# Kernel optimization log

Hardware: AMD Instinct MI355X
Metric: run time of the kernel (lower is better)

Reference implementation:

```python
import jax, jax.numpy as jnp
import numpy as np

BN_EPS = 1e-5


def setup_inputs() -> dict:
    key = jax.random.key(0)
    k1, k2, k3, k4, k5 = jax.random.split(key, 5)
    B, M, N = 4, 65536, 16384
    C_pre, C_cur, D_out = 64, 128, 128
    C_in = C_pre + C_cur  # 192
    pre_x = jax.random.normal(k1, (B, C_pre, M), dtype=jnp.float32)
    cur_x = jax.random.normal(k2, (B, C_cur, N), dtype=jnp.float32)
    up_idx = jax.random.randint(k3, (B, M, 1), 0, N, dtype=jnp.int64)
    w = jax.random.normal(k4, (C_in, D_out), dtype=jnp.float32) * 0.05
    b = jax.random.normal(k5, (D_out,), dtype=jnp.float32) * 0.05
    gamma = jnp.ones((D_out,), dtype=jnp.float32)
    beta = jnp.zeros((D_out,), dtype=jnp.float32)
    run_mean = jnp.zeros((D_out,), dtype=jnp.float32)
    run_var = jnp.ones((D_out,), dtype=jnp.float32)
    return {"pre_x": pre_x, "cur_x": cur_x, "up_idx": up_idx, "w": w, "b": b,
            "gamma": gamma, "beta": beta, "run_mean": run_mean, "run_var": run_var}


def reference(pre_x, cur_x, up_idx, w, b, gamma, beta, run_mean, run_var):
    # indexing_neighbor(cur_x.permute(0,2,1), up_idx).squeeze(2):
    # gather coarse-point features at nearest-neighbor indices -> [B, C_cur, M]
    idx = up_idx[:, :, 0]                                   # [B, M]
    feat = jnp.take_along_axis(cur_x, idx[:, None, :], axis=2)  # [B, C_cur, M]
    x = jnp.concatenate([pre_x, feat], axis=1)              # [B, C_in, M]
    # ConvTranspose1d(kernel=1) == pointwise linear with weight [C_in, D_out]
    y = jnp.einsum('bcm,cd->bdm', x, w) + b[None, :, None]  # [B, D_out, M]
    # BatchNorm1d (inference form with running stats) + ReLU
    inv = jax.lax.rsqrt(run_var + BN_EPS)
    y = (y - run_mean[None, :, None]) * (inv * gamma)[None, :, None] + beta[None, :, None]
    y = jnp.maximum(y, 0.0)
    return y.transpose(0, 2, 1)                             # [B, M, D_out]
```

## Files before the change

### kernel.cpp

```cpp
#include <hip/hip_runtime.h>
#include <hip/hip_bf16.h>


typedef short bhalf8 __attribute__((ext_vector_type(8)));
typedef float f32x4 __attribute__((ext_vector_type(4)));
typedef unsigned int u32x4 __attribute__((ext_vector_type(4)));

__device__ __forceinline__ short f2bf(float f) {
  unsigned int u = __float_as_uint(f);
  unsigned int r = (u + 0x7fffu + ((u >> 16) & 1u)) >> 16;
  return (short)r;
}

__global__ __launch_bounds__(256) void transpose_cur(const float* __restrict__ cur,
                                                     short* __restrict__ curT) {
  __shared__ float tile[128][65];
  const int b = blockIdx.y;
  const int n0 = blockIdx.x << 6;
  const float* src = cur + (size_t)b * 128 * 16384;
#pragma unroll
  for (int it = 0; it < 8; ++it) {
    int v = it * 256 + threadIdx.x;
    int cc = v >> 4;
    int nq = (v & 15) << 2;
    f32x4 f = __builtin_nontemporal_load(
        reinterpret_cast<const f32x4*>(&src[(size_t)cc * 16384 + n0 + nq]));
    tile[cc][nq + 0] = f[0];
    tile[cc][nq + 1] = f[1];
    tile[cc][nq + 2] = f[2];
    tile[cc][nq + 3] = f[3];
  }
  __syncthreads();
  short* dst = curT + ((size_t)b * 16384 + n0) * 128;
#pragma unroll
  for (int it = 0; it < 4; ++it) {
    int v = it * 256 + threadIdx.x;
    int nn = v >> 4;
    int c8 = (v & 15) << 3;
    bhalf8 pk;
#pragma unroll
    for (int j = 0; j < 8; ++j) pk[j] = f2bf(tile[c8 + j][nn]);
    *reinterpret_cast<bhalf8*>(&dst[(size_t)nn * 128 + c8]) = pk;
  }
}

#define NBLK 2048

__global__ __launch_bounds__(256, 3) void fused_gemm(
    const float* __restrict__ pre_x,
    const int* __restrict__ up_idx,
    const float* __restrict__ w,
    const float* __restrict__ bias,
    const float* __restrict__ gamma, const float* __restrict__ beta,
    const float* __restrict__ rmean, const float* __restrict__ rvar,
    const short* __restrict__ curT,
    float* __restrict__ out)
{
  __shared__ short x_lds[64 * 200];
  const int tid = threadIdx.x;
  const int lane = tid & 63;
  const int wv = tid >> 6;
  const int c = lane & 15;
  const int g = lane >> 4;

  bhalf8 bf[6][2];
#pragma unroll
  for (int s = 0; s < 6; ++s)
#pragma unroll
    for (int ct = 0; ct < 2; ++ct) {
      const int col = 32 * wv + 16 * ct + c;
#pragma unroll
      for (int j = 0; j < 8; ++j)
        bf[s][ct][j] = f2bf(w[(32 * s + 8 * g + j) * 128 + col]);
    }

  float scale[2], shift[2];
#pragma unroll
  for (int ct = 0; ct < 2; ++ct) {
    const int d = 32 * wv + 16 * ct + c;
    float sc = gamma[d] * rsqrtf(rvar[d] + 1e-5f);
    scale[ct] = sc;
    shift[ct] = (bias[d] - rmean[d]) * sc + beta[d];
  }

  for (int t = 0; t < 2; ++t) {
    const long rg = blockIdx.x + (long)t * NBLK;
    const long r0 = rg << 6;
    const int b = (int)(r0 >> 16);
    const int m0 = (int)(r0 & 65535);
    if (t) __syncthreads();

    {
      const float* pb = pre_x + (size_t)b * 64 * 65536 + m0;
#pragma unroll
      for (int it = 0; it < 4; ++it) {
        int v = it * 256 + tid;
        int cc = v >> 4;
        int mq = (v & 15) << 2;
        f32x4 f = __builtin_nontemporal_load(
            reinterpret_cast<const f32x4*>(&pb[(size_t)cc * 65536 + mq]));
        x_lds[(mq + 0) * 200 + cc] = f2bf(f[0]);
        x_lds[(mq + 1) * 200 + cc] = f2bf(f[1]);
        x_lds[(mq + 2) * 200 + cc] = f2bf(f[2]);
        x_lds[(mq + 3) * 200 + cc] = f2bf(f[3]);
      }
    }
    {
#pragma unroll
      for (int it = 0; it < 4; ++it) {
        int mm = it * 16 + (tid >> 4);
        int seg = tid & 15;
        int n = up_idx[r0 + mm];
        const short* srcp = curT + ((size_t)b * 16384 + n) * 128 + seg * 8;
        *reinterpret_cast<u32x4*>(&x_lds[mm * 200 + 64 + seg * 8]) =
            *reinterpret_cast<const u32x4*>(srcp);
      }
    }
    __syncthreads();

#pragma unroll
    for (int rt = 0; rt < 4; ++rt) {
      bhalf8 a[6];
#pragma unroll
      for (int s = 0; s < 6; ++s)
        a[s] = *reinterpret_cast<const bhalf8*>(
            &x_lds[(16 * rt + c) * 200 + 32 * s + 8 * g]);
      f32x4 acc0 = {0.f, 0.f, 0.f, 0.f};
      f32x4 acc1 = {0.f, 0.f, 0.f, 0.f};
#pragma unroll
      for (int s = 0; s < 6; ++s) {
        acc0 = __builtin_amdgcn_mfma_f32_16x16x32_bf16(a[s], bf[s][0], acc0, 0, 0, 0);
        acc1 = __builtin_amdgcn_mfma_f32_16x16x32_bf16(a[s], bf[s][1], acc1, 0, 0, 0);
      }
      float* ob = out + (size_t)(r0 + 16 * rt + 4 * g) * 128 + 32 * wv;
#pragma unroll
      for (int i = 0; i < 4; ++i) {
        float v0 = fmaxf(acc0[i] * scale[0] + shift[0], 0.f);
        float v1 = fmaxf(acc1[i] * scale[1] + shift[1], 0.f);
        __builtin_nontemporal_store(v0, ob + (size_t)i * 128 + c);
        __builtin_nontemporal_store(v1, ob + (size_t)i * 128 + 16 + c);
      }
    }
  }
}

extern "C" void kernel_launch(void* const* d_in, const int* in_sizes, int n_in,
                              void* d_out, int out_size, void* d_ws, size_t ws_size,
                              hipStream_t stream) {
  const float* pre_x = (const float*)d_in[0];
  const float* cur_x = (const float*)d_in[1];
  const int* up_idx = (const int*)d_in[2];
  const float* w = (const float*)d_in[3];
  const float* bias = (const float*)d_in[4];
  const float* gamma = (const float*)d_in[5];
  const float* beta = (const float*)d_in[6];
  const float* rmean = (const float*)d_in[7];
  const float* rvar = (const float*)d_in[8];
  float* out = (float*)d_out;
  short* curT = (short*)d_ws;

  hipLaunchKernelGGL(transpose_cur, dim3(256, 4), dim3(256), 0, stream, cur_x, curT);
  hipLaunchKernelGGL(fused_gemm, dim3(NBLK), dim3(256), 0, stream, pre_x, up_idx, w,
                     bias, gamma, beta, rmean, rvar, curT, out);
}
```

Measured before the change: 233.9 us.

## Prefetch second tile into registers and vectorize output stores via swapped MFMA operands

Loads both tiles' indices up front and prefetches the second tile's pre_x and gathered rows into registers while the first tile computes. Swaps the MFMA A/B operands so each lane holds four consecutive output channels, which allows 16-byte vector nontemporal stores in place of scalar ones. BN scale/shift become per-lane vectors to match. Occupancy hint drops from 3 to 2 blocks per CU to make room for the extra prefetch registers.

```diff
diff --git a/kernel.cpp b/kernel.cpp
--- a/kernel.cpp
+++ b/kernel.cpp
@@ -1,5 +1,4 @@
 #include <hip/hip_runtime.h>
-#include <hip/hip_bf16.h>
 
 
 typedef short bhalf8 __attribute__((ext_vector_type(8)));
@@ -46,7 +45,7 @@
 
 #define NBLK 2048
 
-__global__ __launch_bounds__(256, 3) void fused_gemm(
+__global__ __launch_bounds__(256, 2) void fused_gemm(
     const float* __restrict__ pre_x,
     const int* __restrict__ up_idx,
     const float* __restrict__ w,
@@ -62,6 +61,8 @@
   const int wv = tid >> 6;
   const int c = lane & 15;
   const int g = lane >> 4;
+  const int mrow = tid >> 4;
+  const int seg = tid & 15;
 
   bhalf8 bf[6][2];
 #pragma unroll
@@ -74,50 +75,77 @@
         bf[s][ct][j] = f2bf(w[(32 * s + 8 * g + j) * 128 + col]);
     }
 
-  float scale[2], shift[2];
+  f32x4 scale4[2], shift4[2];
 #pragma unroll
   for (int ct = 0; ct < 2; ++ct) {
-    const int d = 32 * wv + 16 * ct + c;
-    float sc = gamma[d] * rsqrtf(rvar[d] + 1e-5f);
-    scale[ct] = sc;
-    shift[ct] = (bias[d] - rmean[d]) * sc + beta[d];
-  }
-
-  for (int t = 0; t < 2; ++t) {
-    const long rg = blockIdx.x + (long)t * NBLK;
-    const long r0 = rg << 6;
-    const int b = (int)(r0 >> 16);
-    const int m0 = (int)(r0 & 65535);
-    if (t) __syncthreads();
-
-    {
-      const float* pb = pre_x + (size_t)b * 64 * 65536 + m0;
-#pragma unroll
-      for (int it = 0; it < 4; ++it) {
-        int v = it * 256 + tid;
-        int cc = v >> 4;
-        int mq = (v & 15) << 2;
-        f32x4 f = __builtin_nontemporal_load(
-            reinterpret_cast<const f32x4*>(&pb[(size_t)cc * 65536 + mq]));
-        x_lds[(mq + 0) * 200 + cc] = f2bf(f[0]);
-        x_lds[(mq + 1) * 200 + cc] = f2bf(f[1]);
-        x_lds[(mq + 2) * 200 + cc] = f2bf(f[2]);
-        x_lds[(mq + 3) * 200 + cc] = f2bf(f[3]);
-      }
+    const int d0 = 32 * wv + 16 * ct + 4 * g;
+    f32x4 gm = *reinterpret_cast<const f32x4*>(&gamma[d0]);
+    f32x4 rv = *reinterpret_cast<const f32x4*>(&rvar[d0]);
+    f32x4 bs = *reinterpret_cast<const f32x4*>(&bias[d0]);
+    f32x4 rm = *reinterpret_cast<const f32x4*>(&rmean[d0]);
+    f32x4 bt = *reinterpret_cast<const f32x4*>(&beta[d0]);
+#pragma unroll
+    for (int i = 0; i < 4; ++i) {
+      float sc = gm[i] * rsqrtf(rv[i] + 1e-5f);
+      scale4[ct][i] = sc;
+      shift4[ct][i] = (bs[i] - rm[i]) * sc + bt[i];
     }
-    {
-#pragma unroll
-      for (int it = 0; it < 4; ++it) {
-        int mm = it * 16 + (tid >> 4);
-        int seg = tid & 15;
-        int n = up_idx[r0 + mm];
-        const short* srcp = curT + ((size_t)b * 16384 + n) * 128 + seg * 8;
-        *reinterpret_cast<u32x4*>(&x_lds[mm * 200 + 64 + seg * 8]) =
-            *reinterpret_cast<const u32x4*>(srcp);
-      }
-    }
-    __syncthreads();
-
+  }
+
+  const long r0a = ((long)blockIdx.x) << 6;
+  const long r0b = ((long)(blockIdx.x + NBLK)) << 6;
+  const int ba = (int)(r0a >> 16), m0a = (int)(r0a & 65535);
+  const int bb = (int)(r0b >> 16), m0b = (int)(r0b & 65535);
+
+  int idx0[4], idx1[4];
+#pragma unroll
+  for (int it = 0; it < 4; ++it) idx0[it] = up_idx[r0a + it * 16 + mrow];
+#pragma unroll
+  for (int it = 0; it < 4; ++it) idx1[it] = up_idx[r0b + it * 16 + mrow];
+
+  f32x4 pre0[4];
+  const float* pba = pre_x + (size_t)ba * 64 * 65536 + m0a;
+#pragma unroll
+  for (int it = 0; it < 4; ++it)
+    pre0[it] = __builtin_nontemporal_load(reinterpret_cast<const f32x4*>(
+        &pba[(size_t)(it * 16 + mrow) * 65536 + (seg << 2)]));
+  u32x4 gat0[4];
+#pragma unroll
+  for (int it = 0; it < 4; ++it)
+    gat0[it] = *reinterpret_cast<const u32x4*>(
+        curT + ((size_t)ba * 16384 + idx0[it]) * 128 + seg * 8);
+
+#define STAGE_LDS(pre, gat)                                                   \
+  {                                                                           \
+    _Pragma("unroll") for (int it = 0; it < 4; ++it) {                        \
+      const int cc = it * 16 + mrow;                                          \
+      const int mq = seg << 2;                                                \
+      x_lds[(mq + 0) * 200 + cc] = f2bf(pre[it][0]);                          \
+      x_lds[(mq + 1) * 200 + cc] = f2bf(pre[it][1]);                          \
+      x_lds[(mq + 2) * 200 + cc] = f2bf(pre[it][2]);                          \
+      x_lds[(mq + 3) * 200 + cc] = f2bf(pre[it][3]);                          \
+    }                                                                         \
+    _Pragma("unroll") for (int it = 0; it < 4; ++it) {                        \
+      const int mm = it * 16 + mrow;                                          \
+      *reinterpret_cast<u32x4*>(&x_lds[mm * 200 + 64 + seg * 8]) = gat[it];   \
+    }                                                                         \
+  }
+
+  STAGE_LDS(pre0, gat0);
+
+  f32x4 pre1[4];
+  const float* pbb = pre_x + (size_t)bb * 64 * 65536 + m0b;
+#pragma unroll
+  for (int it = 0; it < 4; ++it)
+    pre1[it] = __builtin_nontemporal_load(reinterpret_cast<const f32x4*>(
+        &pbb[(size_t)(it * 16 + mrow) * 65536 + (seg << 2)]));
+  u32x4 gat1[4];
+#pragma unroll
+  for (int it = 0; it < 4; ++it)
+    gat1[it] = *reinterpret_cast<const u32x4*>(
+        curT + ((size_t)bb * 16384 + idx1[it]) * 128 + seg * 8);
+
+  auto compute_tile = [&](long r0) {
 #pragma unroll
     for (int rt = 0; rt < 4; ++rt) {
       bhalf8 a[6];
@@ -129,19 +157,27 @@
       f32x4 acc1 = {0.f, 0.f, 0.f, 0.f};
 #pragma unroll
       for (int s = 0; s < 6; ++s) {
-        acc0 = __builtin_amdgcn_mfma_f32_16x16x32_bf16(a[s], bf[s][0], acc0, 0, 0, 0);
-        acc1 = __builtin_amdgcn_mfma_f32_16x16x32_bf16(a[s], bf[s][1], acc1, 0, 0, 0);
+        acc0 = __builtin_amdgcn_mfma_f32_16x16x32_bf16(bf[s][0], a[s], acc0, 0, 0, 0);
+        acc1 = __builtin_amdgcn_mfma_f32_16x16x32_bf16(bf[s][1], a[s], acc1, 0, 0, 0);
       }
-      float* ob = out + (size_t)(r0 + 16 * rt + 4 * g) * 128 + 32 * wv;
+      float* ob = out + (size_t)(r0 + 16 * rt + c) * 128 + 32 * wv + 4 * g;
+      f32x4 v0, v1;
 #pragma unroll
       for (int i = 0; i < 4; ++i) {
-        float v0 = fmaxf(acc0[i] * scale[0] + shift[0], 0.f);
-        float v1 = fmaxf(acc1[i] * scale[1] + shift[1], 0.f);
-        __builtin_nontemporal_store(v0, ob + (size_t)i * 128 + c);
-        __builtin_nontemporal_store(v1, ob + (size_t)i * 128 + 16 + c);
+        v0[i] = fmaxf(acc0[i] * scale4[0][i] + shift4[0][i], 0.f);
+        v1[i] = fmaxf(acc1[i] * scale4[1][i] + shift4[1][i], 0.f);
       }
+      __builtin_nontemporal_store(v0, reinterpret_cast<f32x4*>(ob));
+      __builtin_nontemporal_store(v1, reinterpret_cast<f32x4*>(ob + 16));
     }
-  }
+  };
+
+  __syncthreads();
+  compute_tile(r0a);
+  __syncthreads();
+  STAGE_LDS(pre1, gat1);
+  __syncthreads();
+  compute_tile(r0b);
 }
 
 extern "C" void kernel_launch(void* const* d_in, const int* in_sizes, int n_in,
```

Measured after the change: 255.6 us. 9.3% more time.

## Vectorize output stores via swapped MFMA operands, fold BN scale into weights, prefetch loads

Applied to the files above, without the earlier changes.

Swaps the A/B operands of the MFMA so each lane holds four consecutive output channels of one row, which allows 16-byte nontemporal stores instead of scalar stores. The BN scale is folded into the bf16 weights so the epilogue becomes a single add and ReLU. Index loads for both tiles are hoisted to the start, and the pre_x and gather loads are issued before any LDS writes to overlap memory latency. Occupancy hint is raised to 4 waves per SIMD, and folding the scale before bf16 rounding slightly changes numerics.

```diff
diff --git a/kernel.cpp b/kernel.cpp
--- a/kernel.cpp
+++ b/kernel.cpp
@@ -1,5 +1,4 @@
 #include <hip/hip_runtime.h>
-#include <hip/hip_bf16.h>
 
 
 typedef short bhalf8 __attribute__((ext_vector_type(8)));
@@ -46,7 +45,7 @@
 
 #define NBLK 2048
 
-__global__ __launch_bounds__(256, 3) void fused_gemm(
+__global__ __launch_bounds__(256, 4) void fused_gemm(
     const float* __restrict__ pre_x,
     const int* __restrict__ up_idx,
     const float* __restrict__ w,
@@ -62,6 +61,15 @@
   const int wv = tid >> 6;
   const int c = lane & 15;
   const int g = lane >> 4;
+  const int mrow = tid >> 4;
+  const int seg = tid & 15;
+
+  float scc[2];
+#pragma unroll
+  for (int ct = 0; ct < 2; ++ct) {
+    const int d = 32 * wv + 16 * ct + c;
+    scc[ct] = gamma[d] * rsqrtf(rvar[d] + 1e-5f);
+  }
 
   bhalf8 bf[6][2];
 #pragma unroll
@@ -71,51 +79,63 @@
       const int col = 32 * wv + 16 * ct + c;
 #pragma unroll
       for (int j = 0; j < 8; ++j)
-        bf[s][ct][j] = f2bf(w[(32 * s + 8 * g + j) * 128 + col]);
+        bf[s][ct][j] = f2bf(w[(32 * s + 8 * g + j) * 128 + col] * scc[ct]);
     }
 
-  float scale[2], shift[2];
+  f32x4 shift4[2];
 #pragma unroll
   for (int ct = 0; ct < 2; ++ct) {
-    const int d = 32 * wv + 16 * ct + c;
-    float sc = gamma[d] * rsqrtf(rvar[d] + 1e-5f);
-    scale[ct] = sc;
-    shift[ct] = (bias[d] - rmean[d]) * sc + beta[d];
+    const int d0 = 32 * wv + 16 * ct + 4 * g;
+    f32x4 gm = *reinterpret_cast<const f32x4*>(&gamma[d0]);
+    f32x4 rv = *reinterpret_cast<const f32x4*>(&rvar[d0]);
+    f32x4 bs = *reinterpret_cast<const f32x4*>(&bias[d0]);
+    f32x4 rm = *reinterpret_cast<const f32x4*>(&rmean[d0]);
+    f32x4 bt = *reinterpret_cast<const f32x4*>(&beta[d0]);
+#pragma unroll
+    for (int i = 0; i < 4; ++i) {
+      float sc = gm[i] * rsqrtf(rv[i] + 1e-5f);
+      shift4[ct][i] = (bs[i] - rm[i]) * sc + bt[i];
+    }
+  }
+
+  int idxp[2][4];
+#pragma unroll
+  for (int t = 0; t < 2; ++t) {
+    const long rr = ((long)(blockIdx.x + t * NBLK)) << 6;
+#pragma unroll
+    for (int it = 0; it < 4; ++it) idxp[t][it] = up_idx[rr + it * 16 + mrow];
   }
 
   for (int t = 0; t < 2; ++t) {
-    const long rg = blockIdx.x + (long)t * NBLK;
-    const long r0 = rg << 6;
+    const long r0 = ((long)(blockIdx.x + t * NBLK)) << 6;
     const int b = (int)(r0 >> 16);
     const int m0 = (int)(r0 & 65535);
     if (t) __syncthreads();
 
-    {
-      const float* pb = pre_x + (size_t)b * 64 * 65536 + m0;
+    const float* pb = pre_x + (size_t)b * 64 * 65536 + m0;
+    f32x4 pr[4];
 #pragma unroll
-      for (int it = 0; it < 4; ++it) {
-        int v = it * 256 + tid;
-        int cc = v >> 4;
-        int mq = (v & 15) << 2;
-        f32x4 f = __builtin_nontemporal_load(
-            reinterpret_cast<const f32x4*>(&pb[(size_t)cc * 65536 + mq]));
-        x_lds[(mq + 0) * 200 + cc] = f2bf(f[0]);
-        x_lds[(mq + 1) * 200 + cc] = f2bf(f[1]);
-        x_lds[(mq + 2) * 200 + cc] = f2bf(f[2]);
-        x_lds[(mq + 3) * 200 + cc] = f2bf(f[3]);
-      }
+    for (int it = 0; it < 4; ++it)
+      pr[it] = __builtin_nontemporal_load(reinterpret_cast<const f32x4*>(
+          &pb[(size_t)(it * 16 + mrow) * 65536 + (seg << 2)]));
+    u32x4 gt[4];
+#pragma unroll
+    for (int it = 0; it < 4; ++it)
+      gt[it] = *reinterpret_cast<const u32x4*>(
+          curT + ((size_t)b * 16384 + idxp[t][it]) * 128 + seg * 8);
+#pragma unroll
+    for (int it = 0; it < 4; ++it) {
+      const int cc = it * 16 + mrow;
+      const int mq = seg << 2;
+      x_lds[(mq + 0) * 200 + cc] = f2bf(pr[it][0]);
+      x_lds[(mq + 1) * 200 + cc] = f2bf(pr[it][1]);
+      x_lds[(mq + 2) * 200 + cc] = f2bf(pr[it][2]);
+      x_lds[(mq + 3) * 200 + cc] = f2bf(pr[it][3]);
     }
-    {
 #pragma unroll
-      for (int it = 0; it < 4; ++it) {
-        int mm = it * 16 + (tid >> 4);
-        int seg = tid & 15;
-        int n = up_idx[r0 + mm];
-        const short* srcp = curT + ((size_t)b * 16384 + n) * 128 + seg * 8;
-        *reinterpret_cast<u32x4*>(&x_lds[mm * 200 + 64 + seg * 8]) =
-            *reinterpret_cast<const u32x4*>(srcp);
-      }
-    }
+    for (int it = 0; it < 4; ++it)
+      *reinterpret_cast<u32x4*>(&x_lds[(it * 16 + mrow) * 200 + 64 + seg * 8]) =
+          gt[it];
     __syncthreads();
 
 #pragma unroll
@@ -129,17 +149,18 @@
       f32x4 acc1 = {0.f, 0.f, 0.f, 0.f};
 #pragma unroll
       for (int s = 0; s < 6; ++s) {
-        acc0 = __builtin_amdgcn_mfma_f32_16x16x32_bf16(a[s], bf[s][0], acc0, 0, 0, 0);
-        acc1 = __builtin_amdgcn_mfma_f32_16x16x32_bf16(a[s], bf[s][1], acc1, 0, 0, 0);
+        acc0 = __builtin_amdgcn_mfma_f32_16x16x32_bf16(bf[s][0], a[s], acc0, 0, 0, 0);
+        acc1 = __builtin_amdgcn_mfma_f32_16x16x32_bf16(bf[s][1], a[s], acc1, 0, 0, 0);
       }
-      float* ob = out + (size_t)(r0 + 16 * rt + 4 * g) * 128 + 32 * wv;
+      float* ob = out + (size_t)(r0 + 16 * rt + c) * 128 + 32 * wv + 4 * g;
+      f32x4 v0, v1;
 #pragma unroll
       for (int i = 0; i < 4; ++i) {
-        float v0 = fmaxf(acc0[i] * scale[0] + shift[0], 0.f);
-        float v1 = fmaxf(acc1[i] * scale[1] + shift[1], 0.f);
-        __builtin_nontemporal_store(v0, ob + (size_t)i * 128 + c);
-        __builtin_nontemporal_store(v1, ob + (size_t)i * 128 + 16 + c);
+        v0[i] = fmaxf(acc0[i] + shift4[0][i], 0.f);
+        v1[i] = fmaxf(acc1[i] + shift4[1][i], 0.f);
       }
+      __builtin_nontemporal_store(v0, reinterpret_cast<f32x4*>(ob));
+      __builtin_nontemporal_store(v1, reinterpret_cast<f32x4*>(ob + 16));
     }
   }
 }
```

After: 268.4 us. +14.8%, slower.
